# Kernel tuning notes

Hardware: AMD Instinct MI355X
Metric: run time of the kernel (lower is better)

Reference implementation:

```python
import math
import jax, jax.numpy as jnp
import numpy as np

D_MODEL = 1024
D_FF = 4096
NUM_EXPERTS = 8
CAPACITY_FACTOR = 1.0
ALPHA = 0.01
Z_LOSS_COEF = 0.001
INIT_SCALE = 0.1


def _trunc_normal(key, shape, std, dtype=jnp.float32):
    return jnp.clip(jax.random.normal(key, shape, dtype) * std, -2.0 * std, 2.0 * std)


def setup_inputs() -> dict:
    key = jax.random.key(0)
    kx, kr, k1, k2 = jax.random.split(key, 4)
    x = jax.random.normal(kx, (8, 1024, D_MODEL), jnp.float32)
    # router: nn.Linear(d_model, num_experts, bias=False) -> weight [E, d]
    Wr = _trunc_normal(kr, (NUM_EXPERTS, D_MODEL), math.sqrt(1.0 / D_MODEL) * INIT_SCALE)
    # per-expert FFN: Linear(d, d_ff) -> ReLU -> Linear(d_ff, d)
    W1 = _trunc_normal(k1, (NUM_EXPERTS, D_MODEL, D_FF), math.sqrt(1.0 / D_MODEL) * INIT_SCALE)
    b1 = jnp.zeros((NUM_EXPERTS, D_FF), jnp.float32)
    W2 = _trunc_normal(k2, (NUM_EXPERTS, D_FF, D_MODEL), math.sqrt(1.0 / D_FF) * INIT_SCALE)
    b2 = jnp.zeros((NUM_EXPERTS, D_MODEL), jnp.float32)
    return {"x": x, "Wr": Wr, "W1": W1, "b1": b1, "W2": W2, "b2": b2}


def reference(x, Wr, W1, b1, W2, b2):
    d = x.shape[-1]
    tokens = x.reshape(-1, d)                       # [T, d]
    T = tokens.shape[0]
    E = Wr.shape[0]
    C = max(int(math.ceil(T / float(E) * CAPACITY_FACTOR)), 1)  # expert capacity

    # --- router (eval mode: no dropout, no noise) ---
    logits = tokens @ Wr.T                          # [T, E]
    probs = jax.nn.softmax(logits.astype(jnp.float32), axis=-1)
    top1_prob = jnp.max(probs, axis=-1)             # [T]
    top1_idx = jnp.argmax(probs, axis=-1)           # [T] int

    # --- aux losses (fi uses full top-1 counts, no capacity) ---
    onehot = jax.nn.one_hot(top1_idx, E, dtype=jnp.int32)       # [T, E]
    fi = onehot.sum(axis=0).astype(jnp.float32) / T
    Pi = probs.mean(axis=0)
    aux_loss = ALPHA * E * jnp.dot(fi, Pi)
    aux_loss = aux_loss + Z_LOSS_COEF * jnp.mean(jnp.square(jax.nn.logsumexp(logits, axis=-1)))

    # --- capacity-limited positions (first-come-first-served in token order) ---
    pos_in_bucket = (jnp.cumsum(onehot, axis=0) * onehot).sum(axis=-1) - 1   # [T]
    fits = pos_in_bucket < C                                                 # [T] bool

    # --- dispatch: scatter fitting tokens into [E, C, d]; overflow pos -> OOB -> dropped ---
    scatter_pos = jnp.where(fits, pos_in_bucket, C)
    buf = jnp.zeros((E, C, d), x.dtype).at[top1_idx, scatter_pos].set(tokens, mode='drop')

    # --- per-expert FFN (grouped GEMM) ---
    h = jax.nn.relu(jnp.einsum('ecd,edf->ecf', buf, W1) + b1[:, None, :])    # [E, C, d_ff]
    expert_out = jnp.einsum('ecf,efd->ecd', h, W2) + b2[:, None, :]          # [E, C, d]

    # --- combine: routed tokens get prob-weighted expert output; dropped pass through ---
    gathered = expert_out[top1_idx, jnp.clip(pos_in_bucket, 0, C - 1)]       # [T, d]
    y = jnp.where(fits[:, None], top1_prob[:, None].astype(x.dtype) * gathered, tokens)
    return y.reshape(x.shape), aux_loss
```

## Files before the change

### kernel.cpp

```cpp
#include <hip/hip_runtime.h>

typedef float f32x4 __attribute__((ext_vector_type(4)));
typedef __bf16 bf16x8 __attribute__((ext_vector_type(8)));
typedef unsigned short u16;

__device__ __forceinline__ u16 f2bf(float f) {
  unsigned int u = __builtin_bit_cast(unsigned int, f);
  u += 0x7FFFu + ((u >> 16) & 1u);
  return (u16)(u >> 16);
}

__device__ __forceinline__ void gload16(const void* g, void* l) {
  __builtin_amdgcn_global_load_lds(
      (const __attribute__((address_space(1))) unsigned int*)g,
      (__attribute__((address_space(3))) unsigned int*)l, 16, 0, 0);
}

__global__ __launch_bounds__(256) void kRouter(
    const float* __restrict__ x, const float* __restrict__ Wr,
    int* __restrict__ tok_e, float* __restrict__ tok_p,
    float* __restrict__ partials ) {
  __shared__ float wr[8192];
  __shared__ float red[4][12];
  int tid = threadIdx.x;
#pragma unroll
  for (int i = 0; i < 8; ++i)
    *(float4*)&wr[tid * 4 + i * 1024] = *(const float4*)&Wr[tid * 4 + i * 1024];
  __syncthreads();
  int w = tid >> 6, lane = tid & 63;
  int t = blockIdx.x * 4 + w;
  const float* xp = x + (size_t)t * 1024;
  float acc[8];
#pragma unroll
  for (int e = 0; e < 8; ++e) acc[e] = 0.f;
#pragma unroll
  for (int i = 0; i < 8; ++i) {
    float2 xv = *(const float2*)&xp[i * 128 + lane * 2];
#pragma unroll
    for (int e = 0; e < 8; ++e) {
      float2 wv = *(const float2*)&wr[e * 1024 + i * 128 + lane * 2];
      acc[e] += xv.x * wv.x + xv.y * wv.y;
    }
  }
#pragma unroll
  for (int off = 32; off; off >>= 1) {
#pragma unroll
    for (int e = 0; e < 8; ++e) acc[e] += __shfl_xor(acc[e], off, 64);
  }
  int bi = 0;
  float m = acc[0];
#pragma unroll
  for (int e = 1; e < 8; ++e)
    if (acc[e] > m) { m = acc[e]; bi = e; }
  float ex[8], s = 0.f;
#pragma unroll
  for (int e = 0; e < 8; ++e) { ex[e] = expf(acc[e] - m); s += ex[e]; }
  float inv = 1.f / s;
  float lse = m + logf(s);
  if (lane == 0) {
    tok_e[t] = bi;
    tok_p[t] = inv;
#pragma unroll
    for (int e = 0; e < 8; ++e) red[w][e] = ex[e] * inv;
    red[w][8] = lse * lse;
  }
  __syncthreads();
  if (tid < 9) {
    float v = red[0][tid] + red[1][tid] + red[2][tid] + red[3][tid];
    partials[tid * 2048 + blockIdx.x] = v;
  }
}

__global__ __launch_bounds__(256) void kScan(
    const int* __restrict__ tok_e, const float* __restrict__ tok_p,
    const float* __restrict__ partials,
    int* __restrict__ tok_row, int* __restrict__ row2tok,
    float* __restrict__ row_prob, int* __restrict__ cnt_arr,
    float* __restrict__ aux_out) {
  __shared__ int sc[8][256];
  __shared__ float fr[256];
  __shared__ int tot[8];
  __shared__ float ps[9];
  int tid = threadIdx.x;
  int base = tid * 32;
  int lc[8];
#pragma unroll
  for (int e = 0; e < 8; ++e) lc[e] = 0;
  for (int j = 0; j < 32; ++j) lc[tok_e[base + j]]++;
#pragma unroll
  for (int e = 0; e < 8; ++e) sc[e][tid] = lc[e];
  __syncthreads();
  for (int s = 1; s < 256; s <<= 1) {
    int v[8];
#pragma unroll
    for (int e = 0; e < 8; ++e) v[e] = (tid >= s) ? sc[e][tid - s] : 0;
    __syncthreads();
#pragma unroll
    for (int e = 0; e < 8; ++e) sc[e][tid] += v[e];
    __syncthreads();
  }
  if (tid < 8) {
    tot[tid] = sc[tid][255];
    cnt_arr[tid] = min(sc[tid][255], 1024);
  }
  for (int c = 0; c < 9; ++c) {
    float sl = 0.f;
    for (int i = tid; i < 2048; i += 256) sl += partials[c * 2048 + i];
    fr[tid] = sl;
    __syncthreads();
    for (int s2 = 128; s2; s2 >>= 1) {
      if (tid < s2) fr[tid] += fr[tid + s2];
      __syncthreads();
    }
    if (tid == 0) ps[c] = fr[0];
    __syncthreads();
  }
  if (tid == 0) {
    float dot = 0.f;
#pragma unroll
    for (int e = 0; e < 8; ++e)
      dot += ((float)tot[e] / 8192.f) * (ps[e] / 8192.f);
    aux_out[0] = 0.01f * 8.f * dot + 0.001f * (ps[8] / 8192.f);
  }
  int run[8];
#pragma unroll
  for (int e = 0; e < 8; ++e) run[e] = sc[e][tid] - lc[e];
  for (int j = 0; j < 32; ++j) {
    int t = base + j;
    int e = tok_e[t];
    int p = run[e]++;
    if (p < 1024) {
      int row = e * 1024 + p;
      tok_row[t] = row;
      row2tok[row] = t;
      row_prob[row] = tok_p[t];
    } else {
      tok_row[t] = -1;
    }
  }
}

__global__ __launch_bounds__(256) void kDispatch(
    const float* __restrict__ x, const int* __restrict__ tok_row,
    u16* __restrict__ Xd, float* __restrict__ y) {
  int t = blockIdx.x, tid = threadIdx.x;
  int row = tok_row[t];
  float4 v = *(const float4*)&x[(size_t)t * 1024 + tid * 4];
  if (row >= 0) {
    ushort4 o;
    o.x = f2bf(v.x); o.y = f2bf(v.y); o.z = f2bf(v.z); o.w = f2bf(v.w);
    *(ushort4*)&Xd[(size_t)row * 1024 + tid * 4] = o;
  } else {
    *(float4*)&y[(size_t)t * 1024 + tid * 4] = v;
  }
}

__global__ __launch_bounds__(256) void kTransConv(
    const float* __restrict__ src, u16* __restrict__ dst, int K, int N) {
  __shared__ u16 tl[64 * 66];
  int e = blockIdx.z;
  int n0 = blockIdx.x * 64, k0 = blockIdx.y * 64;
  src += (size_t)e * K * N;
  dst += (size_t)e * N * K;
  int tid = threadIdx.x;
  int rk = tid >> 4;
  int rn = (tid & 15) * 4;
#pragma unroll
  for (int j = 0; j < 4; ++j) {
    int k = rk + j * 16;
    float4 v = *(const float4*)&src[(size_t)(k0 + k) * N + n0 + rn];
    tl[(rn + 0) * 66 + k] = f2bf(v.x);
    tl[(rn + 1) * 66 + k] = f2bf(v.y);
    tl[(rn + 2) * 66 + k] = f2bf(v.z);
    tl[(rn + 3) * 66 + k] = f2bf(v.w);
  }
  __syncthreads();
  int f = tid >> 2;
  int seg = (tid & 3) * 16;
  uint4 tv[2];
  u16* tp = (u16*)tv;
#pragma unroll
  for (int i = 0; i < 16; ++i) tp[i] = tl[f * 66 + seg + i];
  *(uint4*)&dst[(size_t)(n0 + f) * K + k0 + seg] = tv[0];
  *(uint4*)&dst[(size_t)(n0 + f) * K + k0 + seg + 8] = tv[1];
}

template <int MODE>
__global__ __launch_bounds__(256) void kGemm(
    const u16* __restrict__ A, const u16* __restrict__ B,
    const float* __restrict__ bias,
    u16* __restrict__ Hout, float* __restrict__ Yout,
    const int* __restrict__ cnt_arr, const int* __restrict__ row2tok,
    const float* __restrict__ row_prob, int K, int N) {
  int e = blockIdx.z, mt = blockIdx.y, nt = blockIdx.x;
  int cnt = cnt_arr[e];
  if (mt * 128 >= cnt) return;
  __shared__ u16 As[128 * 32];
  __shared__ u16 Bs[128 * 32];
  int tid = threadIdx.x, lane = tid & 63, w = tid >> 6;
  int wr = w >> 1, wc = w & 1, lrow = lane & 15, kg = lane >> 4;
  const u16* Ab = A + (size_t)(e * 1024 + mt * 128) * K;
  const u16* Bb = B + (size_t)e * N * K + (size_t)(nt * 128) * K;
  f32x4 acc[4][4];
#pragma unroll
  for (int i = 0; i < 4; ++i)
#pragma unroll
    for (int j = 0; j < 4; ++j) acc[i][j] = (f32x4)0.f;
  int i0 = (w * 2) * 64 + lane;
  int i1 = i0 + 64;
  int r0 = i0 >> 2, ks0 = (i0 & 3) * 8;
  int r1 = i1 >> 2, ks1 = (i1 & 3) * 8;
  for (int k0 = 0; k0 < K; k0 += 32) {
    gload16(Ab + (size_t)r0 * K + k0 + ks0, &As[i0 * 8]);
    gload16(Ab + (size_t)r1 * K + k0 + ks1, &As[i1 * 8]);
    gload16(Bb + (size_t)r0 * K + k0 + ks0, &Bs[i0 * 8]);
    gload16(Bb + (size_t)r1 * K + k0 + ks1, &Bs[i1 * 8]);
    __syncthreads();
    bf16x8 a[4], b[4];
#pragma unroll
    for (int mi = 0; mi < 4; ++mi)
      a[mi] = *(const bf16x8*)&As[(wr * 64 + mi * 16 + lrow) * 32 + kg * 8];
#pragma unroll
    for (int ni = 0; ni < 4; ++ni)
      b[ni] = *(const bf16x8*)&Bs[(wc * 64 + ni * 16 + lrow) * 32 + kg * 8];
#pragma unroll
    for (int mi = 0; mi < 4; ++mi)
#pragma unroll
      for (int ni = 0; ni < 4; ++ni)
        acc[mi][ni] = __builtin_amdgcn_mfma_f32_16x16x32_bf16(
            a[mi], b[ni], acc[mi][ni], 0, 0, 0);
    __syncthreads();
  }
  int n0 = nt * 128;
  if (MODE == 1) {
#pragma unroll
    for (int ni = 0; ni < 4; ++ni) {
      int col = n0 + wc * 64 + ni * 16 + lrow;
      float bv = bias[e * N + col];
#pragma unroll
      for (int mi = 0; mi < 4; ++mi)
#pragma unroll
        for (int j = 0; j < 4; ++j) {
          int rl = wr * 64 + mi * 16 + kg * 4 + j;
          float v = fmaxf(acc[mi][ni][j] + bv, 0.f);
          Hout[(size_t)(e * 1024 + mt * 128 + rl) * N + col] = f2bf(v);
        }
    }
  } else {
    int cols[4];
    float bv[4];
#pragma unroll
    for (int ni = 0; ni < 4; ++ni) {
      cols[ni] = n0 + wc * 64 + ni * 16 + lrow;
      bv[ni] = bias[e * N + cols[ni]];
    }
#pragma unroll
    for (int mi = 0; mi < 4; ++mi)
#pragma unroll
      for (int j = 0; j < 4; ++j) {
        int rl = wr * 64 + mi * 16 + kg * 4 + j;
        int rie = mt * 128 + rl;
        if (rie < cnt) {
          int grow = e * 1024 + rie;
          int tt = row2tok[grow];
          float pp = row_prob[grow];
          float* yr = Yout + (size_t)tt * 1024;
#pragma unroll
          for (int ni = 0; ni < 4; ++ni)
            yr[cols[ni]] = pp * (acc[mi][ni][j] + bv[ni]);
        }
      }
  }
}

extern "C" void kernel_launch(void* const* d_in, const int* in_sizes, int n_in,
                              void* d_out, int out_size, void* d_ws, size_t ws_size,
                              hipStream_t stream) {
  (void)in_sizes; (void)n_in; (void)out_size; (void)ws_size;
  const float* x  = (const float*)d_in[0];
  const float* Wr = (const float*)d_in[1];
  const float* W1 = (const float*)d_in[2];
  const float* b1 = (const float*)d_in[3];
  const float* W2 = (const float*)d_in[4];
  const float* b2 = (const float*)d_in[5];
  float* y = (float*)d_out;
  char* ws = (char*)d_ws;
  u16*   W1T      = (u16*)(ws);
  u16*   W2T      = (u16*)(ws + 67108864);
  u16*   Xd       = (u16*)(ws + 134217728);
  u16*   H        = (u16*)(ws + 150994944);
  int*   tok_e    = (int*)(ws + 218103808);
  float* tok_p    = (float*)(ws + 218136576);
  int*   tok_row  = (int*)(ws + 218169344);
  int*   row2tok  = (int*)(ws + 218202112);
  float* row_prob = (float*)(ws + 218234880);
  int*   cnt_arr  = (int*)(ws + 218267648);
  float* partials = (float*)(ws + 218267776);

  kRouter<<<2048, 256, 0, stream>>>(x, Wr, tok_e, tok_p, partials);
  kScan<<<1, 256, 0, stream>>>(tok_e, tok_p, partials, tok_row, row2tok,
                               row_prob, cnt_arr, y + 8388608);
  kDispatch<<<8192, 256, 0, stream>>>(x, tok_row, Xd, y);
  kTransConv<<<dim3(64, 16, 8), 256, 0, stream>>>(W1, W1T, 1024, 4096);
  kTransConv<<<dim3(16, 64, 8), 256, 0, stream>>>(W2, W2T, 4096, 1024);
  kGemm<1><<<dim3(32, 8, 8), 256, 0, stream>>>(Xd, W1T, b1, H, nullptr,
                                               cnt_arr, nullptr, nullptr, 1024, 4096);
  kGemm<2><<<dim3(8, 8, 8), 256, 0, stream>>>(H, W2T, b2, nullptr, y,
                                              cnt_arr, row2tok, row_prob, 4096, 1024);
}
```

Baseline: 635.4 us.

## Rewrite expert GEMMs as 256x256 double-buffered 8-wave kernels with split-K combine

Replaces the simple 128x128 single-buffered GEMM with a 512-thread, 256x256-tile kernel using XOR-swizzled LDS, double-buffered direct-to-LDS loads interleaved with MFMA quarters, explicit barriers/waitcnt and setprio. The second GEMM is split along K into two halves writing fp32 partials into the (now dead) W1T workspace, followed by a new combine kernel that adds the partials and bias, applies the prob and scatters to tokens. This aims to raise MFMA utilisation and hide global load latency, at the cost of extra partial-buffer traffic, an additional launch, and fragile hand-placed synchronisation.

```diff
diff --git a/kernel.cpp b/kernel.cpp
--- a/kernel.cpp
+++ b/kernel.cpp
@@ -15,6 +15,12 @@
       (const __attribute__((address_space(1))) unsigned int*)g,
       (__attribute__((address_space(3))) unsigned int*)l, 16, 0, 0);
 }
+
+#define BAR()   asm volatile("s_barrier" ::: "memory")
+#define LGKM0() asm volatile("s_waitcnt lgkmcnt(0)" ::: "memory")
+#define VMCNT6() asm volatile("s_waitcnt vmcnt(6)" ::: "memory")
+#define PRIO1 __builtin_amdgcn_s_setprio(1)
+#define PRIO0 __builtin_amdgcn_s_setprio(0)
 
 __global__ __launch_bounds__(256) void kRouter(
     const float* __restrict__ x, const float* __restrict__ Wr,
@@ -185,92 +191,177 @@
   *(uint4*)&dst[(size_t)(n0 + f) * K + k0 + seg + 8] = tv[1];
 }
 
+
+#define STA(BUF, U, KK) do {                                                       \
+    int ra0_ = (U) * 64 + (tid >> 3);                                              \
+    int ra1_ = 128 + ra0_;                                                         \
+    gload16(Atb + (size_t)ra0_ * KD + (KK) + csw, &smA[BUF][ra0_ * 64 + dsl]);     \
+    gload16(Atb + (size_t)ra1_ * KD + (KK) + csw, &smA[BUF][ra1_ * 64 + dsl]);     \
+  } while (0)
+
+#define BROW(RIDX, U) ((((RIDX) >> 5) * 64) + (U) * 32 + ((RIDX) & 31))
+#define STB(BUF, U, KK) do {                                                       \
+    int rb0_ = BROW(tid >> 3, U);                                                  \
+    int rb1_ = BROW(64 + (tid >> 3), U);                                           \
+    gload16(Btb + (size_t)rb0_ * KD + (KK) + csw, &smB[BUF][rb0_ * 64 + dsl]);     \
+    gload16(Btb + (size_t)rb1_ * KD + (KK) + csw, &smB[BUF][rb1_ * 64 + dsl]);     \
+  } while (0)
+
+#define LDA(MB, BUF) do {                                                          \
+    _Pragma("unroll") for (int m_ = 0; m_ < 4; ++m_)                               \
+    _Pragma("unroll") for (int ks_ = 0; ks_ < 2; ++ks_)                            \
+      av[m_][ks_] = *(const bf16x8*)&smA[BUF][(aro + ((MB) + m_) * 16) * 64 + cofs[ks_]]; \
+  } while (0)
+
+#define LDB(DST, NB, BUF) do {                                                     \
+    _Pragma("unroll") for (int n_ = 0; n_ < 2; ++n_)                               \
+    _Pragma("unroll") for (int ks_ = 0; ks_ < 2; ++ks_)                            \
+      DST[n_][ks_] = *(const bf16x8*)&smB[BUF][(bro + ((NB) + n_) * 16) * 64 + cofs[ks_]]; \
+  } while (0)
+
+#define MFMAQ(MB, BV, NB) do {                                                     \
+    _Pragma("unroll") for (int m_ = 0; m_ < 4; ++m_)                               \
+    _Pragma("unroll") for (int n_ = 0; n_ < 2; ++n_)                               \
+    _Pragma("unroll") for (int ks_ = 0; ks_ < 2; ++ks_)                            \
+      acc[(MB) + m_][(NB) + n_] = __builtin_amdgcn_mfma_f32_16x16x32_bf16(         \
+          av[m_][ks_], BV[n_][ks_], acc[(MB) + m_][(NB) + n_], 0, 0, 0);           \
+  } while (0)
+
 template <int MODE>
-__global__ __launch_bounds__(256) void kGemm(
-    const u16* __restrict__ A, const u16* __restrict__ B,
-    const float* __restrict__ bias,
-    u16* __restrict__ Hout, float* __restrict__ Yout,
-    const int* __restrict__ cnt_arr, const int* __restrict__ row2tok,
-    const float* __restrict__ row_prob, int K, int N) {
-  int e = blockIdx.z, mt = blockIdx.y, nt = blockIdx.x;
-  int cnt = cnt_arr[e];
-  if (mt * 128 >= cnt) return;
-  __shared__ u16 As[128 * 32];
-  __shared__ u16 Bs[128 * 32];
-  int tid = threadIdx.x, lane = tid & 63, w = tid >> 6;
-  int wr = w >> 1, wc = w & 1, lrow = lane & 15, kg = lane >> 4;
-  const u16* Ab = A + (size_t)(e * 1024 + mt * 128) * K;
-  const u16* Bb = B + (size_t)e * N * K + (size_t)(nt * 128) * K;
-  f32x4 acc[4][4];
-#pragma unroll
-  for (int i = 0; i < 4; ++i)
+__global__ __launch_bounds__(512, 2) void kGemm8(
+    const u16* __restrict__ A, const u16* __restrict__ Bw,
+    const float* __restrict__ bias, u16* __restrict__ Hout,
+    float* __restrict__ Pout, const int* __restrict__ cnt_arr) {
+  constexpr int KD = (MODE == 1) ? 1024 : 4096;
+  constexpr int ND = (MODE == 1) ? 4096 : 1024;
+  constexpr int NT = (MODE == 1) ? 16 : 32;
+  __shared__ u16 smA[2][16384];
+  __shared__ u16 smB[2][16384];
+  const int nt = blockIdx.x;
+  const int mt = blockIdx.y;
+  const int e  = (MODE == 1) ? blockIdx.z : (blockIdx.z >> 1);
+  const int kbase = (MODE == 1) ? 0 : ((blockIdx.z & 1) * 2048);
+  const int cnt = cnt_arr[e];
+  if (mt * 256 >= cnt) return;
+  const int tid = threadIdx.x;
+  const int lane = tid & 63, wid = tid >> 6;
+  const int wr = wid >> 2, wc = wid & 3;
+  const int lrow = lane & 15, kg = lane >> 4;
+  const u16* Atb = A + (size_t)(e * 1024 + mt * 256) * KD + kbase;
+  const u16* Btb = Bw + (size_t)e * ND * KD + (size_t)(nt * 256) * KD + kbase;
+  const int csw = (((tid & 7) ^ ((tid >> 3) & 7))) * 8;
+  const int dsl = (tid & 7) * 8;
+  const int aro = wr * 128 + lrow;
+  const int bro = wc * 64 + lrow;
+  const int sw = lrow & 7;
+  const int cofs[2] = { ((0 + kg) ^ sw) * 8, ((4 + kg) ^ sw) * 8 };
+
+  f32x4 acc[8][4];
+#pragma unroll
+  for (int i = 0; i < 8; ++i)
 #pragma unroll
     for (int j = 0; j < 4; ++j) acc[i][j] = (f32x4)0.f;
-  int i0 = (w * 2) * 64 + lane;
-  int i1 = i0 + 64;
-  int r0 = i0 >> 2, ks0 = (i0 & 3) * 8;
-  int r1 = i1 >> 2, ks1 = (i1 & 3) * 8;
-  for (int k0 = 0; k0 < K; k0 += 32) {
-    gload16(Ab + (size_t)r0 * K + k0 + ks0, &As[i0 * 8]);
-    gload16(Ab + (size_t)r1 * K + k0 + ks1, &As[i1 * 8]);
-    gload16(Bb + (size_t)r0 * K + k0 + ks0, &Bs[i0 * 8]);
-    gload16(Bb + (size_t)r1 * K + k0 + ks1, &Bs[i1 * 8]);
-    __syncthreads();
-    bf16x8 a[4], b[4];
-#pragma unroll
-    for (int mi = 0; mi < 4; ++mi)
-      a[mi] = *(const bf16x8*)&As[(wr * 64 + mi * 16 + lrow) * 32 + kg * 8];
-#pragma unroll
-    for (int ni = 0; ni < 4; ++ni)
-      b[ni] = *(const bf16x8*)&Bs[(wc * 64 + ni * 16 + lrow) * 32 + kg * 8];
-#pragma unroll
-    for (int mi = 0; mi < 4; ++mi)
-#pragma unroll
-      for (int ni = 0; ni < 4; ++ni)
-        acc[mi][ni] = __builtin_amdgcn_mfma_f32_16x16x32_bf16(
-            a[mi], b[ni], acc[mi][ni], 0, 0, 0);
-    __syncthreads();
-  }
-  int n0 = nt * 128;
+  bf16x8 av[4][2], b0[2][2], b1[2][2];
+
+  STA(0, 0, 0); STB(0, 0, 0); STB(0, 1, 0); STA(0, 1, 0);
+  STA(1, 0, 64); STB(1, 0, 64); STB(1, 1, 64);
+  VMCNT6();
+  BAR();
+
+  for (int i = 0; i < NT / 2; ++i) {
+    const int kc1 = (2 * i + 1) * 64;
+    const int kn  = (2 * i + 2 < NT) ? (2 * i + 2) * 64 : 0;
+    const int kn1 = (2 * i + 3 < NT) ? (2 * i + 3) * 64 : 0;
+    LDA(0, 0); LDB(b0, 0, 0);
+    STA(1, 1, kc1);
+    BAR(); LGKM0();
+    PRIO1; MFMAQ(0, b0, 0); PRIO0;
+    BAR();
+    LDB(b1, 2, 0);
+    STA(0, 0, kn);
+    BAR(); LGKM0();
+    PRIO1; MFMAQ(0, b1, 2); PRIO0;
+    BAR();
+    LDA(4, 0);
+    STB(0, 0, kn);
+    BAR(); LGKM0();
+    PRIO1; MFMAQ(4, b0, 0); PRIO0;
+    BAR();
+    STB(0, 1, kn);
+    VMCNT6();
+    BAR();
+    PRIO1; MFMAQ(4, b1, 2); PRIO0;
+    BAR();
+    LDA(0, 1); LDB(b0, 0, 1);
+    STA(0, 1, kn);
+    BAR(); LGKM0();
+    PRIO1; MFMAQ(0, b0, 0); PRIO0;
+    BAR();
+    LDB(b1, 2, 1);
+    STA(1, 0, kn1);
+    BAR(); LGKM0();
+    PRIO1; MFMAQ(0, b1, 2); PRIO0;
+    BAR();
+    LDA(4, 1);
+    STB(1, 0, kn1);
+    BAR(); LGKM0();
+    PRIO1; MFMAQ(4, b0, 0); PRIO0;
+    BAR();
+    STB(1, 1, kn1);
+    VMCNT6();
+    BAR();
+    PRIO1; MFMAQ(4, b1, 2); PRIO0;
+    BAR();
+  }
+
+  const int colb = nt * 256 + wc * 64 + lrow;
   if (MODE == 1) {
-#pragma unroll
-    for (int ni = 0; ni < 4; ++ni) {
-      int col = n0 + wc * 64 + ni * 16 + lrow;
-      float bv = bias[e * N + col];
-#pragma unroll
-      for (int mi = 0; mi < 4; ++mi)
-#pragma unroll
-        for (int j = 0; j < 4; ++j) {
-          int rl = wr * 64 + mi * 16 + kg * 4 + j;
-          float v = fmaxf(acc[mi][ni][j] + bv, 0.f);
-          Hout[(size_t)(e * 1024 + mt * 128 + rl) * N + col] = f2bf(v);
-        }
-    }
+    float bv[4];
+#pragma unroll
+    for (int ni = 0; ni < 4; ++ni) bv[ni] = bias[e * 4096 + colb + ni * 16];
+#pragma unroll
+    for (int mi = 0; mi < 8; ++mi)
+#pragma unroll
+      for (int jj = 0; jj < 4; ++jj) {
+        size_t rbase = (size_t)(e * 1024 + mt * 256 + wr * 128 + mi * 16 + kg * 4 + jj) * 4096;
+#pragma unroll
+        for (int ni = 0; ni < 4; ++ni)
+          Hout[rbase + colb + ni * 16] = f2bf(fmaxf(acc[mi][ni][jj] + bv[ni], 0.f));
+      }
   } else {
-    int cols[4];
-    float bv[4];
-#pragma unroll
-    for (int ni = 0; ni < 4; ++ni) {
-      cols[ni] = n0 + wc * 64 + ni * 16 + lrow;
-      bv[ni] = bias[e * N + cols[ni]];
-    }
-#pragma unroll
-    for (int mi = 0; mi < 4; ++mi)
-#pragma unroll
-      for (int j = 0; j < 4; ++j) {
-        int rl = wr * 64 + mi * 16 + kg * 4 + j;
-        int rie = mt * 128 + rl;
-        if (rie < cnt) {
-          int grow = e * 1024 + rie;
-          int tt = row2tok[grow];
-          float pp = row_prob[grow];
-          float* yr = Yout + (size_t)tt * 1024;
-#pragma unroll
-          for (int ni = 0; ni < 4; ++ni)
-            yr[cols[ni]] = pp * (acc[mi][ni][j] + bv[ni]);
-        }
+    float* P = Pout + (size_t)(blockIdx.z & 1) * 8388608;
+#pragma unroll
+    for (int mi = 0; mi < 8; ++mi)
+#pragma unroll
+      for (int jj = 0; jj < 4; ++jj) {
+        size_t rbase = (size_t)(e * 1024 + mt * 256 + wr * 128 + mi * 16 + kg * 4 + jj) * 1024;
+#pragma unroll
+        for (int ni = 0; ni < 4; ++ni)
+          P[rbase + colb + ni * 16] = acc[mi][ni][jj];
       }
   }
+}
+
+__global__ __launch_bounds__(256) void kCombine(
+    const float* __restrict__ P0, const float* __restrict__ P1,
+    const float* __restrict__ b2, const int* __restrict__ cnt_arr,
+    const int* __restrict__ row2tok, const float* __restrict__ row_prob,
+    float* __restrict__ y) {
+  int r = blockIdx.x;
+  int e = r >> 10, rie = r & 1023;
+  if (rie >= cnt_arr[e]) return;
+  int tok = row2tok[r];
+  float pp = row_prob[r];
+  int c = threadIdx.x * 4;
+  float4 p0 = *(const float4*)&P0[(size_t)r * 1024 + c];
+  float4 p1 = *(const float4*)&P1[(size_t)r * 1024 + c];
+  float4 bb = *(const float4*)&b2[e * 1024 + c];
+  float4 o;
+  o.x = pp * (p0.x + p1.x + bb.x);
+  o.y = pp * (p0.y + p1.y + bb.y);
+  o.z = pp * (p0.z + p1.z + bb.z);
+  o.w = pp * (p0.w + p1.w + bb.w);
+  *(float4*)&y[(size_t)tok * 1024 + c] = o;
 }
 
 extern "C" void kernel_launch(void* const* d_in, const int* in_sizes, int n_in,
@@ -296,6 +387,7 @@
   float* row_prob = (float*)(ws + 218234880);
   int*   cnt_arr  = (int*)(ws + 218267648);
   float* partials = (float*)(ws + 218267776);
+  float* Pbuf     = (float*)ws;
 
   kRouter<<<2048, 256, 0, stream>>>(x, Wr, tok_e, tok_p, partials);
   kScan<<<1, 256, 0, stream>>>(tok_e, tok_p, partials, tok_row, row2tok,
@@ -303,8 +395,8 @@
   kDispatch<<<8192, 256, 0, stream>>>(x, tok_row, Xd, y);
   kTransConv<<<dim3(64, 16, 8), 256, 0, stream>>>(W1, W1T, 1024, 4096);
   kTransConv<<<dim3(16, 64, 8), 256, 0, stream>>>(W2, W2T, 4096, 1024);
-  kGemm<1><<<dim3(32, 8, 8), 256, 0, stream>>>(Xd, W1T, b1, H, nullptr,
-                                               cnt_arr, nullptr, nullptr, 1024, 4096);
-  kGemm<2><<<dim3(8, 8, 8), 256, 0, stream>>>(H, W2T, b2, nullptr, y,
-                                              cnt_arr, row2tok, row_prob, 4096, 1024);
-}
+  kGemm8<1><<<dim3(16, 4, 8), 512, 0, stream>>>(Xd, W1T, b1, H, nullptr, cnt_arr);
+  kGemm8<2><<<dim3(4, 4, 16), 512, 0, stream>>>(H, W2T, nullptr, nullptr, Pbuf, cnt_arr);
+  kCombine<<<8192, 256, 0, stream>>>(Pbuf, Pbuf + 8388608, b2, cnt_arr,
+                                     row2tok, row_prob, y);
+}
```

Result: faster. 571.5 us (-10.1%).
